# Performance work log

Hardware: AMD Instinct MI355X
Metric: run time of the kernel (lower is better)

## Reference

```python
import jax, jax.numpy as jnp
import numpy as np
from math import pi

B, L, S, D, H, M, DK, IND, KS = 8, 3072, 3072, 512, 8, 2, 64, 96, 25


def _linear(x, W, b):
    return x @ W + b


def _moving_avg(x, k):
    # Autoformer-style moving average with edge replication, stride 1.  x: [B, T, D]
    pad = (k - 1) // 2
    xp = jnp.concatenate([jnp.repeat(x[:, :1], pad, axis=1), x,
                          jnp.repeat(x[:, -1:], pad, axis=1)], axis=1)
    c = jnp.cumsum(xp, axis=1)
    c = jnp.concatenate([jnp.zeros_like(c[:, :1]), c], axis=1)
    return (c[:, k:] - c[:, :-k]) / k


def _trend_norm(x, g, b):
    # series_decomp(kernel=25): LayerNorm the seasonal part, add back the trend.
    trend = _moving_avg(x, KS)
    seas = x - trend
    mu = jnp.mean(seas, axis=-1, keepdims=True)
    var = jnp.var(seas, axis=-1, keepdims=True)
    return (seas - mu) * jax.lax.rsqrt(var + 1e-5) * g + b + trend


def _quat_attention(q, k, v, q_om, q_th, k_om, k_th):
    # q: [B,Lq,H,E]; k,v: [B,Sk,H,E]; omegas/thetas: [B,*,H,M]
    Bq, Lq, Hh, E = q.shape
    Sk = k.shape[1]
    Mm = q_om.shape[-1]
    qpos = (jnp.arange(Lq, dtype=q.dtype) / Lq)[None, :, None, None]
    kpos = (jnp.arange(Sk, dtype=q.dtype) / Sk)[None, :, None, None]
    Qa = q_om * qpos + q_th
    Ka = k_om * kpos + k_th
    Qc, Qs = jnp.cos(Qa), jnp.sin(Qa)
    Kc, Ks = jnp.cos(Ka), jnp.sin(Ka)
    q0, q1, q2, q3 = jnp.split(q, 4, axis=-1)
    k0, k1, k2, k3 = jnp.split(k, 4, axis=-1)
    op = lambda a, t: jnp.einsum('blhe,blhm->blhme', a, t)
    Qr = jnp.concatenate([op(q0, Qc) - op(q1, Qs), op(q1, Qc) + op(q0, Qs),
                          op(q2, Qc) + op(q3, Qs), op(q3, Qc) - op(q2, Qs)], axis=-1)
    Kr = jnp.concatenate([op(k0, Kc) - op(k2, Ks), op(k1, Kc) - op(k3, Ks),
                          op(k2, Kc) + op(k0, Ks), op(k3, Kc) + op(k1, Ks)], axis=-1)
    scores = jnp.einsum('blhme,bshme->bhls', Qr, Kr) / Mm
    scale = 1.0 / jnp.sqrt(jnp.asarray(E, q.dtype))
    A = jax.nn.softmax(scale * scores, axis=-1)
    return jnp.einsum('bhls,bshd->blhd', A, v)


def _ltr_layer(p, queries, keys, values):
    Bq, Lq, _ = queries.shape
    Sk = keys.shape[1]
    # kernel_size=1 convs == pointwise linears
    q_om = jax.nn.relu(_linear(queries, p['Wqo'], p['bqo'])).reshape(Bq, Lq, H, M)
    k_om = jax.nn.relu(_linear(keys, p['Wko'], p['bko'])).reshape(Bq, Sk, H, M)
    q_th = (jnp.tanh(_linear(queries, p['Wqt'], p['bqt'])) * pi).reshape(Bq, Lq, H, M)
    k_th = (jnp.tanh(_linear(keys, p['Wkt'], p['bkt'])) * pi).reshape(Bq, Sk, H, M)
    q = _linear(queries, p['Wq'], p['bq']).reshape(Bq, Lq, H, DK)
    k = _linear(keys, p['Wk'], p['bk']).reshape(Bq, Sk, H, DK)
    v = _linear(values, p['Wv'], p['bv']).reshape(Bq, Sk, H, DK)
    out = _quat_attention(q, k, v, q_om, q_th, k_om, k_th).reshape(Bq, Lq, H * DK)
    # D-matrix penalty == first-order difference along sequence
    om_pen = jnp.sum(jnp.diff(q_om, axis=1) ** 2) + jnp.sum(jnp.diff(k_om, axis=1) ** 2)
    th_pen = jnp.sum(q_th ** 2) + jnp.sum(k_th ** 2)
    return _linear(out, p['Wo'], p['bo']), om_pen, th_pen


def setup_inputs() -> dict:
    key = jax.random.key(0)
    ks = iter(jax.random.split(key, 32))
    rn = lambda shape, s=1.0: jax.random.normal(next(ks), shape, jnp.float32) * s
    w = 0.03  # ~1/sqrt(d_model)
    return dict(
        queries=rn((B, L, D)), keys=rn((B, S, D)), values=rn((B, S, D)),
        Wq=rn((2, D, D), w), bq=jnp.zeros((2, D), jnp.float32),
        Wk=rn((2, D, D), w), bk=jnp.zeros((2, D), jnp.float32),
        Wv=rn((2, D, D), w), bv=jnp.zeros((2, D), jnp.float32),
        Wqo=rn((2, D, M * H), w), bqo=jnp.zeros((2, M * H), jnp.float32),
        Wko=rn((2, D, M * H), w), bko=jnp.zeros((2, M * H), jnp.float32),
        Wqt=rn((2, D, M * H), w), bqt=jnp.zeros((2, M * H), jnp.float32),
        Wkt=rn((2, D, M * H), w), bkt=jnp.zeros((2, M * H), jnp.float32),
        Wo=rn((2, D, D), w), bo=jnp.zeros((2, D), jnp.float32),
        I=rn((1, IND, D), w),
        ln_g=jnp.ones((D,), jnp.float32), ln_b=jnp.zeros((D,), jnp.float32),
    )


def reference(queries, keys, values, Wq, bq, Wk, bk, Wv, bv, Wqo, bqo, Wko, bko,
              Wqt, bqt, Wkt, bkt, Wo, bo, I, ln_g, ln_b):
    def lp(i):
        return dict(Wq=Wq[i], bq=bq[i], Wk=Wk[i], bk=bk[i], Wv=Wv[i], bv=bv[i],
                    Wqo=Wqo[i], bqo=bqo[i], Wko=Wko[i], bko=bko[i],
                    Wqt=Wqt[i], bqt=bqt[i], Wkt=Wkt[i], bkt=bkt[i],
                    Wo=Wo[i], bo=bo[i])
    Bq = queries.shape[0]
    inducings = jnp.broadcast_to(I, (Bq, IND, D))
    inducings, om1, th1 = _ltr_layer(lp(0), inducings, keys, values)
    inducings = _trend_norm(inducings, ln_g, ln_b)
    out, om2, th2 = _ltr_layer(lp(1), queries, inducings, inducings)
    return out, om1 + om2, th1 + th2
```

## Files before the change

### kernel.cpp

```cpp
#include <hip/hip_runtime.h>
#include <math.h>

#define PI_F 3.14159265358979323846f

namespace {
constexpr int B_ = 8;
constexpr int L_ = 3072;
constexpr int S_ = 3072;
constexpr int H_ = 8;
constexpr int NF = 544;
constexpr int NSC = 8;
constexpr int SCHUNK = S_ / NSC;
}

typedef __attribute__((ext_vector_type(8))) short bf16x8;
typedef __attribute__((ext_vector_type(4))) float f32x4;

__device__ inline f32x4 mfma16(bf16x8 a, bf16x8 b, f32x4 c) {
  return __builtin_amdgcn_mfma_f32_16x16x32_bf16(a, b, c, 0, 0, 0);
}

__device__ inline ushort f2bf(float f) {
  union { float f; unsigned u; } v;
  v.f = f;
  unsigned r = v.u + 0x7FFFu + ((v.u >> 16) & 1u);
  return (ushort)(r >> 16);
}

__device__ inline void gl_lds16(const void* g, void* l) {
  __builtin_amdgcn_global_load_lds(
      (const __attribute__((address_space(1))) unsigned int*)g,
      (__attribute__((address_space(3))) unsigned int*)l, 16, 0, 0);
}

__device__ inline int xcd_swizzle(int flat, int nwg) {
  int q = nwg >> 3, r = nwg & 7;
  int xcd = flat & 7, ix = flat >> 3;
  return (xcd < r ? xcd * (q + 1) : r * (q + 1) + (xcd - r) * q) + ix;
}

__global__ void init_pen(float* pen) {
  if (threadIdx.x < 16) pen[threadIdx.x] = 0.f;
}

__global__ void write_pen(const float* __restrict__ pen, float* __restrict__ out) {
  if (threadIdx.x == 0) out[12582912] = pen[0];
  if (threadIdx.x == 1) out[12582913] = pen[1];
}

__global__ void pack_w(const float* __restrict__ Wm, const float* __restrict__ Wo_,
                       const float* __restrict__ Wt, const float* __restrict__ bm,
                       const float* __restrict__ bo_, const float* __restrict__ bt,
                       float* __restrict__ Wcat, float* __restrict__ bcat) {
  int gid = blockIdx.x * 256 + threadIdx.x;
  if (gid < 512 * 544) {
    int k = gid / 544, n = gid % 544;
    float v;
    if (n < 512) v = Wm[(size_t)k * 512 + n];
    else if (n < 528) v = Wo_[k * 16 + (n - 512)];
    else v = Wt[k * 16 + (n - 528)];
    Wcat[gid] = v;
  }
  if (gid < 544) {
    float v;
    if (gid < 512) v = bm[gid];
    else if (gid < 528) v = bo_[gid - 512];
    else v = bt[gid - 528];
    bcat[gid] = v;
  }
}

__global__ void pack_wt_fused(const float* __restrict__ Wm, const float* __restrict__ Wo_,
                              const float* __restrict__ Wt, const float* __restrict__ bm,
                              const float* __restrict__ bo_, const float* __restrict__ bt,
                              ushort* __restrict__ BT, float* __restrict__ bias) {
  int gid = blockIdx.x * 256 + threadIdx.x;
  if (gid < 640 * 512) {
    int n = gid >> 9, k = gid & 511;
    float v = 0.f;
    if (n < 512) v = Wm[(size_t)k * 512 + n];
    else if (n < 528) v = Wo_[k * 16 + (n - 512)];
    else if (n < 544) v = Wt[k * 16 + (n - 528)];
    BT[gid] = f2bf(v);
  }
  if (gid < 544)
    bias[gid] = (gid < 512) ? bm[gid] : (gid < 528 ? bo_[gid - 512] : bt[gid - 528]);
}

__global__ void pack_wt_plain(const float* __restrict__ W, const float* __restrict__ b,
                              ushort* __restrict__ BT, float* __restrict__ bias) {
  int gid = blockIdx.x * 256 + threadIdx.x;
  if (gid < 512 * 512) {
    int n = gid >> 9, k = gid & 511;
    BT[gid] = f2bf(W[(size_t)k * 512 + n]);
  }
  if (gid < 512) bias[gid] = b[gid];
}

__global__ __launch_bounds__(256)
void cast_bf16(const float* __restrict__ src, ushort* __restrict__ dst, int n8) {
  int gid = blockIdx.x * 256 + threadIdx.x;
  if (gid < n8) {
    float4 a = ((const float4*)src)[(size_t)gid * 2];
    float4 b = ((const float4*)src)[(size_t)gid * 2 + 1];
    ushort u[8] = {f2bf(a.x), f2bf(a.y), f2bf(a.z), f2bf(a.w),
                   f2bf(b.x), f2bf(b.y), f2bf(b.z), f2bf(b.w)};
    ((uint4*)dst)[gid] = *(uint4*)u;
  }
}

__global__ __launch_bounds__(256)
void gemm_bf16_mfma(const ushort* __restrict__ A, const ushort* __restrict__ BT,
                    const float* __restrict__ bias, float* __restrict__ C,
                    int ldc, int Nout, int act) {
  __shared__ ushort As[128][32];
  __shared__ ushort Bs[128][32];
  const int tid = threadIdx.x;
  const int wv = tid >> 6, lane = tid & 63, quad = lane >> 4, col = lane & 15;
  const int wm = wv & 1, wn = wv >> 1;

  const int nwg = gridDim.x * gridDim.y;
  const int flat = blockIdx.y * gridDim.x + blockIdx.x;
  const int nf = xcd_swizzle(flat, nwg);
  const int bx = nf % gridDim.x, by = nf / gridDim.x;
  const int m0 = by * 128, n0 = bx * 128;

  const int srow = lane >> 2;
  const int scol = (lane & 3) * 8;

  f32x4 acc[4][4];
#pragma unroll
  for (int i = 0; i < 4; ++i)
#pragma unroll
    for (int j = 0; j < 4; ++j) {
      f32x4 z = {0.f, 0.f, 0.f, 0.f};
      acc[i][j] = z;
    }

  const ushort* Ag = A + (size_t)(m0 + wv * 32) * 512;
  const ushort* Bg = BT + (size_t)(n0 + wv * 32) * 512;

  for (int k0 = 0; k0 < 512; k0 += 32) {
    __syncthreads();
    gl_lds16(Ag + (size_t)srow * 512 + k0 + scol, &As[wv * 32][0]);
    gl_lds16(Ag + (size_t)(srow + 16) * 512 + k0 + scol, &As[wv * 32 + 16][0]);
    gl_lds16(Bg + (size_t)srow * 512 + k0 + scol, &Bs[wv * 32][0]);
    gl_lds16(Bg + (size_t)(srow + 16) * 512 + k0 + scol, &Bs[wv * 32 + 16][0]);
    __syncthreads();
    bf16x8 av[4], bv[4];
#pragma unroll
    for (int mi = 0; mi < 4; ++mi)
      av[mi] = *(const bf16x8*)&As[wm * 64 + mi * 16 + col][quad * 8];
#pragma unroll
    for (int ni = 0; ni < 4; ++ni)
      bv[ni] = *(const bf16x8*)&Bs[wn * 64 + ni * 16 + col][quad * 8];
#pragma unroll
    for (int mi = 0; mi < 4; ++mi)
#pragma unroll
      for (int ni = 0; ni < 4; ++ni)
        acc[mi][ni] = mfma16(av[mi], bv[ni], acc[mi][ni]);
  }

#pragma unroll
  for (int mi = 0; mi < 4; ++mi) {
#pragma unroll
    for (int ni = 0; ni < 4; ++ni) {
      int n = n0 + wn * 64 + ni * 16 + col;
      if (n >= Nout) continue;
      float bs = bias[n];
#pragma unroll
      for (int r = 0; r < 4; ++r) {
        int m = m0 + wm * 64 + mi * 16 + quad * 4 + r;
        float v = acc[mi][ni][r] + bs;
        if (act && n >= 512) v = (n < 528) ? fmaxf(v, 0.f) : tanhf(v) * PI_F;
        C[(size_t)m * ldc + n] = v;
      }
    }
  }
}

__global__ __launch_bounds__(256)
void gemm_k512(const float* __restrict__ A, const float* __restrict__ W,
               const float* __restrict__ bias, float* __restrict__ C,
               int M, int N, int act) {
  __shared__ float As[16][68];
  __shared__ float Ws_[16][68];
  const int tid = threadIdx.x;
  const int tx = tid & 15, ty = tid >> 4;
  const int m0 = blockIdx.y * 64, n0 = blockIdx.x * 64;

  float acc[4][4];
#pragma unroll
  for (int i = 0; i < 4; ++i)
#pragma unroll
    for (int j = 0; j < 4; ++j) acc[i][j] = 0.f;

  const int arow = tid >> 2;
  const int acol4 = (tid & 3) * 4;
  const int wrow = tid >> 4;
  const int wcol4 = (tid & 15) * 4;

  for (int k0 = 0; k0 < 512; k0 += 16) {
    float4 av = make_float4(0.f, 0.f, 0.f, 0.f);
    int gm = m0 + arow;
    if (gm < M) av = *(const float4*)(A + (size_t)gm * 512 + k0 + acol4);
    As[acol4 + 0][arow] = av.x;
    As[acol4 + 1][arow] = av.y;
    As[acol4 + 2][arow] = av.z;
    As[acol4 + 3][arow] = av.w;
    float4 wv;
    int gn = n0 + wcol4;
    if (gn + 3 < N) {
      wv = *(const float4*)(W + (size_t)(k0 + wrow) * N + gn);
    } else {
      float tmp[4] = {0.f, 0.f, 0.f, 0.f};
      for (int u = 0; u < 4; ++u)
        if (gn + u < N) tmp[u] = W[(size_t)(k0 + wrow) * N + gn + u];
      wv = make_float4(tmp[0], tmp[1], tmp[2], tmp[3]);
    }
    *(float4*)&Ws_[wrow][wcol4] = wv;
    __syncthreads();
#pragma unroll
    for (int k = 0; k < 16; ++k) {
      float4 a4 = *(const float4*)&As[k][ty * 4];
      float4 b4 = *(const float4*)&Ws_[k][tx * 4];
      float a[4] = {a4.x, a4.y, a4.z, a4.w};
      float b[4] = {b4.x, b4.y, b4.z, b4.w};
#pragma unroll
      for (int i = 0; i < 4; ++i)
#pragma unroll
        for (int j = 0; j < 4; ++j) acc[i][j] = fmaf(a[i], b[j], acc[i][j]);
    }
    __syncthreads();
  }

#pragma unroll
  for (int i = 0; i < 4; ++i) {
    int gm = m0 + ty * 4 + i;
    if (gm >= M) continue;
#pragma unroll
    for (int j = 0; j < 4; ++j) {
      int gn = n0 + tx * 4 + j;
      if (gn >= N) continue;
      float v = acc[i][j] + bias[gn];
      if (act && gn >= 512) v = (gn < 528) ? fmaxf(v, 0.f) : tanhf(v) * PI_F;
      C[(size_t)gm * N + gn] = v;
    }
  }
}

__global__ __launch_bounds__(256)
void build_qr0(const float* __restrict__ QF0, ushort* __restrict__ Qr0bf) {
  const int l = blockIdx.x;
  const float* row = QF0 + (size_t)l * NF;
  __shared__ float2 trig[8][2];
  const int tid = threadIdx.x;
  if (tid < 16) {
    int h = tid >> 1, m = tid & 1;
    float om = row[512 + h * 2 + m], th = row[528 + h * 2 + m];
    float qa = fmaf(om, (float)l / 96.f, th);
    trig[h][m] = make_float2(cosf(qa), sinf(qa));
  }
  __syncthreads();
  for (int idx = tid; idx < 1024; idx += 256) {
    int h = idx >> 7, d = idx & 127;
    int m = d >> 6, r = d & 63, c = r >> 4, e = r & 15;
    float qc = row[h * 64 + c * 16 + e];
    float qp = row[h * 64 + (c ^ 1) * 16 + e];
    float2 tg = trig[h][m];
    float sgn = (c == 0 || c == 3) ? -1.f : 1.f;
    Qr0bf[((size_t)h * 96 + l) * 128 + d] = f2bf(fmaf(qc, tg.x, sgn * qp * tg.y));
  }
}

__global__ __launch_bounds__(256)
void build_kr0(const float* __restrict__ KF0, ushort* __restrict__ Kr0) {
  const int rs = blockIdx.x;
  const int b = rs / S_, s = rs - b * S_;
  const float* row = KF0 + (size_t)rs * NF;
  __shared__ float2 trig[8][2];
  const int tid = threadIdx.x;
  if (tid < 16) {
    int h = tid >> 1, m = tid & 1;
    float om = row[512 + h * 2 + m], th = row[528 + h * 2 + m];
    float ka = fmaf(om, (float)s * (1.f / (float)S_), th);
    trig[h][m] = make_float2(cosf(ka), sinf(ka));
  }
  __syncthreads();
  for (int idx = tid; idx < 512; idx += 256) {
    int h = idx >> 6, d = (idx & 63) * 2;
    int m = d >> 6, r = d & 63, c = r >> 4, e = r & 15;
    const float* rh = row + h * 64;
    float2 kc = *(const float2*)(rh + c * 16 + e);
    float2 kp = *(const float2*)(rh + (c ^ 2) * 16 + e);
    float2 tg = trig[h][m];
    float sgn = (c < 2) ? -1.f : 1.f;
    ushort2 u;
    u.x = f2bf(fmaf(kc.x, tg.x, sgn * kp.x * tg.y));
    u.y = f2bf(fmaf(kc.y, tg.x, sgn * kp.y * tg.y));
    *(ushort2*)&Kr0[(((size_t)(b * 8 + h)) * S_ + s) * 128 + d] = u;
  }
}

__global__ __launch_bounds__(256)
void build_vt0(const float* __restrict__ V0, ushort* __restrict__ Vt0) {
  const int st = blockIdx.x, h = blockIdx.y, b = blockIdx.z;
  const int s0 = st * 64;
  const int tid = threadIdx.x;
  __shared__ ushort T[64][68];
  for (int idx = tid; idx < 4096; idx += 256) {
    int s = idx >> 6, d = idx & 63;
    T[d][s] = f2bf(V0[((size_t)(b * S_ + s0 + s)) * 512 + h * 64 + d]);
  }
  __syncthreads();
  for (int idx = tid; idx < 2048; idx += 256) {
    int d = idx >> 5, s2 = (idx & 31) * 2;
    ushort2 u = *(const ushort2*)&T[d][s2];
    *(ushort2*)&Vt0[(((size_t)(b * 8 + h)) * 64 + d) * S_ + s0 + s2] = u;
  }
}

__global__ __launch_bounds__(256)
void build_kr1(const float* __restrict__ KF1, float* __restrict__ Kr1) {
  const int rs = blockIdx.x;
  const int b = rs / 96, s = rs % 96;
  const float* row = KF1 + (size_t)rs * NF;
  __shared__ float2 trig[8][2];
  const int tid = threadIdx.x;
  if (tid < 16) {
    int h = tid >> 1, m = tid & 1;
    float om = row[512 + h * 2 + m], th = row[528 + h * 2 + m];
    float ka = fmaf(om, (float)s / 96.f, th);
    trig[h][m] = make_float2(cosf(ka), sinf(ka));
  }
  __syncthreads();
  for (int idx = tid; idx < 1024; idx += 256) {
    int h = idx >> 7, d = idx & 127;
    int m = d >> 6, r = d & 63, c = r >> 4, e = r & 15;
    float kc = row[h * 64 + c * 16 + e];
    float kp = row[h * 64 + (c ^ 2) * 16 + e];
    float2 tg = trig[h][m];
    float sgn = (c < 2) ? -1.f : 1.f;
    Kr1[(((size_t)(b * 8 + h)) * 96 + s) * 128 + d] = fmaf(kc, tg.x, sgn * kp * tg.y);
  }
}

__global__ __launch_bounds__(256)
void attn0_mfma(const ushort* __restrict__ Kr0, const ushort* __restrict__ Vt0,
                const ushort* __restrict__ Qr0bf, float* __restrict__ accP,
                float* __restrict__ sumP) {
  const int sc = blockIdx.x, h = blockIdx.y, b = blockIdx.z;
  const int tid = threadIdx.x;
  const int wv = tid >> 6, lane = tid & 63, quad = lane >> 4, col = lane & 15;

  __shared__ __align__(16) ushort Qs[96][136];
  __shared__ __align__(16) ushort Ks[64][136];
  __shared__ __align__(16) ushort Vt[64][72];
  __shared__ __align__(16) ushort Ps[96][72];
  __shared__ float rowsum[96];

  const ushort* Qg = Qr0bf + (size_t)h * 96 * 128;
  for (int idx = tid; idx < 96 * 16; idx += 256) {
    int l = idx >> 4, c8 = (idx & 15) * 8;
    *(uint4*)&Qs[l][c8] = *(const uint4*)(Qg + (size_t)l * 128 + c8);
  }
  if (tid < 96) rowsum[tid] = 0.f;

  f32x4 oacc[6];
#pragma unroll
  for (int i = 0; i < 6; ++i) {
    f32x4 z = {0.f, 0.f, 0.f, 0.f};
    oacc[i] = z;
  }

  const int s0g = sc * SCHUNK;
  const ushort* Kb = Kr0 + ((size_t)(b * 8 + h) * S_ + s0g) * 128;
  const ushort* Vb = Vt0 + ((size_t)(b * 8 + h)) * 64 * S_ + s0g;

  for (int t = 0; t < 6; ++t) {
    __syncthreads();
    for (int idx = tid; idx < 64 * 16; idx += 256) {
      int s = idx >> 4, c8 = (idx & 15) * 8;
      *(uint4*)&Ks[s][c8] = *(const uint4*)(Kb + ((size_t)(t * 64 + s)) * 128 + c8);
    }
    for (int idx = tid; idx < 64 * 8; idx += 256) {
      int d = idx >> 3, c8 = (idx & 7) * 8;
      *(uint4*)&Vt[d][c8] = *(const uint4*)(Vb + (size_t)d * S_ + t * 64 + c8);
    }
    __syncthreads();
    bf16x8 bk[4];
#pragma unroll
    for (int k = 0; k < 4; ++k)
      bk[k] = *(const bf16x8*)&Ks[wv * 16 + col][k * 32 + quad * 8];
    f32x4 sacc[6];
#pragma unroll
    for (int mt = 0; mt < 6; ++mt) {
      f32x4 z = {0.f, 0.f, 0.f, 0.f};
      sacc[mt] = z;
#pragma unroll
      for (int k = 0; k < 4; ++k) {
        bf16x8 a = *(const bf16x8*)&Qs[mt * 16 + col][k * 32 + quad * 8];
        sacc[mt] = mfma16(a, bk[k], sacc[mt]);
      }
    }
#pragma unroll
    for (int mt = 0; mt < 6; ++mt) {
      float pr[4];
#pragma unroll
      for (int r = 0; r < 4; ++r) {
        float p = __expf(sacc[mt][r] * 0.0625f);
        pr[r] = p;
        Ps[mt * 16 + quad * 4 + r][wv * 16 + col] = f2bf(p);
      }
#pragma unroll
      for (int r = 0; r < 4; ++r) {
#pragma unroll
        for (int off = 1; off < 16; off <<= 1) pr[r] += __shfl_xor(pr[r], off);
      }
      if (col == 0) {
#pragma unroll
        for (int r = 0; r < 4; ++r)
          atomicAdd(&rowsum[mt * 16 + quad * 4 + r], pr[r]);
      }
    }
    __syncthreads();
    bf16x8 bv0 = *(const bf16x8*)&Vt[wv * 16 + col][quad * 8];
    bf16x8 bv1 = *(const bf16x8*)&Vt[wv * 16 + col][32 + quad * 8];
#pragma unroll
    for (int mt = 0; mt < 6; ++mt) {
      bf16x8 a0 = *(const bf16x8*)&Ps[mt * 16 + col][quad * 8];
      oacc[mt] = mfma16(a0, bv0, oacc[mt]);
      bf16x8 a1 = *(const bf16x8*)&Ps[mt * 16 + col][32 + quad * 8];
      oacc[mt] = mfma16(a1, bv1, oacc[mt]);
    }
  }
  __syncthreads();
  const size_t pbase = (((size_t)(b * 8 + h)) * NSC + sc) * 96;
#pragma unroll
  for (int mt = 0; mt < 6; ++mt) {
#pragma unroll
    for (int r = 0; r < 4; ++r) {
      int l = mt * 16 + quad * 4 + r;
      accP[(pbase + l) * 64 + wv * 16 + col] = oacc[mt][r];
    }
  }
  if (tid < 96) sumP[pbase + tid] = rowsum[tid];
}

__global__ __launch_bounds__(256)
void attn0_stage2(const float* __restrict__ accP, const float* __restrict__ sumP,
                  float* __restrict__ attn0) {
  const int l = blockIdx.x, b = blockIdx.y;
  const int tid = threadIdx.x;
  for (int e = tid; e < 512; e += 256) {
    int h = e >> 6, d = e & 63;
    size_t base = ((size_t)(b * 8 + h)) * NSC * 96;
    float num = 0.f, den = 0.f;
    for (int scv = 0; scv < NSC; ++scv) {
      size_t pb = base + (size_t)scv * 96 + l;
      num += accP[pb * 64 + d];
      den += sumP[pb];
    }
    attn0[((size_t)(b * 96 + l)) * 512 + e] = num / den;
  }
}

__global__ __launch_bounds__(256)
void trend_norm(const float* __restrict__ y, const float* __restrict__ g,
                const float* __restrict__ be, float* __restrict__ outp) {
  const int t = blockIdx.x, b = blockIdx.y;
  const int tid = threadIdx.x;
  __shared__ float red[256];
  __shared__ float red2[256];
  float seas[2], trend[2];
  float lsum = 0.f, lsum2 = 0.f;
#pragma unroll
  for (int u = 0; u < 2; ++u) {
    int d = tid + u * 256;
    float tr = 0.f;
    for (int j = -12; j <= 12; ++j) {
      int tt = t + j;
      tt = tt < 0 ? 0 : (tt > 95 ? 95 : tt);
      tr += y[((size_t)(b * 96 + tt)) * 512 + d];
    }
    tr *= (1.f / 25.f);
    float x = y[((size_t)(b * 96 + t)) * 512 + d];
    float se = x - tr;
    seas[u] = se;
    trend[u] = tr;
    lsum += se;
    lsum2 += se * se;
  }
  red[tid] = lsum;
  red2[tid] = lsum2;
  __syncthreads();
  for (int off = 128; off > 0; off >>= 1) {
    if (tid < off) {
      red[tid] += red[tid + off];
      red2[tid] += red2[tid + off];
    }
    __syncthreads();
  }
  float mu = red[0] / 512.f;
  float var = red2[0] / 512.f - mu * mu;
  float rs = rsqrtf(var + 1e-5f);
#pragma unroll
  for (int u = 0; u < 2; ++u) {
    int d = tid + u * 256;
    outp[((size_t)(b * 96 + t)) * 512 + d] = (seas[u] - mu) * rs * g[d] + be[d] + trend[u];
  }
}

__global__ __launch_bounds__(256)
void penalty(const float* __restrict__ base, int R, int nb, float mult,
             float* __restrict__ pen) {
  const int tid = threadIdx.x;
  size_t gid = (size_t)blockIdx.x * 256 + tid;
  size_t total = (size_t)nb * R * 16;
  float omv = 0.f, thv = 0.f;
  if (gid < total) {
    int j = (int)(gid & 15);
    size_t row = gid >> 4;
    int s = (int)(row % R);
    const float* r0 = base + row * NF;
    float th = r0[528 + j];
    thv = th * th;
    if (s < R - 1) {
      float d = r0[NF + 512 + j] - r0[512 + j];
      omv = d * d;
    }
  }
  __shared__ float ro[256], rt[256];
  ro[tid] = omv;
  rt[tid] = thv;
  __syncthreads();
  for (int off = 128; off > 0; off >>= 1) {
    if (tid < off) {
      ro[tid] += ro[tid + off];
      rt[tid] += rt[tid + off];
    }
    __syncthreads();
  }
  if (tid == 0) {
    atomicAdd(pen + 0, mult * ro[0]);
    atomicAdd(pen + 1, mult * rt[0]);
  }
}

__global__ __launch_bounds__(256)
void attn1_mfma(const float* __restrict__ QF1, const float* __restrict__ Kr1,
                const float* __restrict__ V1, ushort* __restrict__ attn1) {
  const int nwg = gridDim.x * gridDim.y * gridDim.z;
  const int flat = (blockIdx.z * gridDim.y + blockIdx.y) * gridDim.x + blockIdx.x;
  const int nf = xcd_swizzle(flat, nwg);
  const int lt = nf % gridDim.x;
  const int rest = nf / gridDim.x;
  const int h = rest % gridDim.y, b = rest / gridDim.y;
  const int l0 = lt * 64;
  const int tid = threadIdx.x;
  const int wv = tid >> 6, lane = tid & 63, quad = lane >> 4, col = lane & 15;

  __shared__ __align__(16) ushort Qs[64][136];
  __shared__ __align__(16) ushort Ks[96][136];
  __shared__ __align__(16) ushort Vt[64][104];
  __shared__ __align__(16) ushort Ps[64][104];
  __shared__ float2 trigq[64][2];

  if (tid < 128) {
    int l = tid >> 1, m = tid & 1;
    const float* row = QF1 + (size_t)(b * L_ + l0 + l) * NF;
    float om = row[512 + h * 2 + m];
    float th = row[528 + h * 2 + m];
    float qa = fmaf(om, (float)(l0 + l) * (1.f / (float)L_), th);
    trigq[l][m] = make_float2(cosf(qa), sinf(qa));
  }
  __syncthreads();
  for (int idx = tid; idx < 64 * 128; idx += 256) {
    int l = idx >> 7, d = idx & 127;
    int m = d >> 6, r = d & 63, c = r >> 4, e = r & 15;
    const float* row = QF1 + (size_t)(b * L_ + l0 + l) * NF + h * 64;
    float qc = row[c * 16 + e];
    float qp = row[(c ^ 1) * 16 + e];
    float2 tg = trigq[l][m];
    float sgn = (c == 0 || c == 3) ? -1.f : 1.f;
    Qs[l][d] = f2bf(fmaf(qc, tg.x, sgn * qp * tg.y));
  }
  const float* Krb = Kr1 + (size_t)(b * 8 + h) * 96 * 128;
  for (int idx = tid; idx < 96 * 64; idx += 256) {
    int s = idx >> 6, d2 = (idx & 63) * 2;
    float2 kk = *(const float2*)(Krb + (size_t)s * 128 + d2);
    ushort2 u;
    u.x = f2bf(kk.x);
    u.y = f2bf(kk.y);
    *(ushort2*)&Ks[s][d2] = u;
  }
  for (int idx = tid; idx < 96 * 64; idx += 256) {
    int s = idx >> 6, d = idx & 63;
    Vt[d][s] = f2bf(V1[(size_t)(b * 96 + s) * 512 + h * 64 + d]);
  }
  __syncthreads();

  bf16x8 aq[4];
#pragma unroll
  for (int k = 0; k < 4; ++k)
    aq[k] = *(const bf16x8*)&Qs[wv * 16 + col][k * 32 + quad * 8];
  f32x4 sacc[6];
#pragma unroll
  for (int nt = 0; nt < 6; ++nt) {
    f32x4 z = {0.f, 0.f, 0.f, 0.f};
    sacc[nt] = z;
#pragma unroll
    for (int k = 0; k < 4; ++k) {
      bf16x8 bkf = *(const bf16x8*)&Ks[nt * 16 + col][k * 32 + quad * 8];
      sacc[nt] = mfma16(aq[k], bkf, sacc[nt]);
    }
  }
  float rsum[4] = {0.f, 0.f, 0.f, 0.f};
#pragma unroll
  for (int nt = 0; nt < 6; ++nt) {
#pragma unroll
    for (int r = 0; r < 4; ++r) {
      float p = __expf(sacc[nt][r] * 0.0625f);
      Ps[wv * 16 + quad * 4 + r][nt * 16 + col] = f2bf(p);
      rsum[r] += p;
    }
  }
#pragma unroll
  for (int r = 0; r < 4; ++r) {
#pragma unroll
    for (int off = 1; off < 16; off <<= 1) rsum[r] += __shfl_xor(rsum[r], off);
  }
  __syncthreads();
  bf16x8 ap[3];
#pragma unroll
  for (int kt = 0; kt < 3; ++kt)
    ap[kt] = *(const bf16x8*)&Ps[wv * 16 + col][kt * 32 + quad * 8];
  f32x4 oacc[4];
#pragma unroll
  for (int nt = 0; nt < 4; ++nt) {
    f32x4 z = {0.f, 0.f, 0.f, 0.f};
    oacc[nt] = z;
#pragma unroll
    for (int kt = 0; kt < 3; ++kt) {
      bf16x8 bvf = *(const bf16x8*)&Vt[nt * 16 + col][kt * 32 + quad * 8];
      oacc[nt] = mfma16(ap[kt], bvf, oacc[nt]);
    }
  }
  float inv[4];
#pragma unroll
  for (int r = 0; r < 4; ++r) inv[r] = 1.f / rsum[r];
#pragma unroll
  for (int nt = 0; nt < 4; ++nt) {
#pragma unroll
    for (int r = 0; r < 4; ++r) {
      int l = wv * 16 + quad * 4 + r;
      attn1[(size_t)(b * L_ + l0 + l) * 512 + h * 64 + nt * 16 + col] =
          f2bf(oacc[nt][r] * inv[r]);
    }
  }
}

extern "C" void kernel_launch(void* const* d_in, const int* in_sizes, int n_in,
                              void* d_out, int out_size, void* d_ws, size_t ws_size,
                              hipStream_t stream) {
  (void)in_sizes; (void)n_in; (void)out_size; (void)ws_size;
  const float* queries = (const float*)d_in[0];
  const float* keys = (const float*)d_in[1];
  const float* values = (const float*)d_in[2];
  const float* Wq = (const float*)d_in[3];
  const float* bq = (const float*)d_in[4];
  const float* Wk = (const float*)d_in[5];
  const float* bk = (const float*)d_in[6];
  const float* Wv = (const float*)d_in[7];
  const float* bv = (const float*)d_in[8];
  const float* Wqo = (const float*)d_in[9];
  const float* bqo = (const float*)d_in[10];
  const float* Wko = (const float*)d_in[11];
  const float* bko = (const float*)d_in[12];
  const float* Wqt = (const float*)d_in[13];
  const float* bqt = (const float*)d_in[14];
  const float* Wkt = (const float*)d_in[15];
  const float* bkt = (const float*)d_in[16];
  const float* Wo = (const float*)d_in[17];
  const float* bo = (const float*)d_in[18];
  const float* I = (const float*)d_in[19];
  const float* ln_g = (const float*)d_in[20];
  const float* ln_b = (const float*)d_in[21];
  float* out = (float*)d_out;

  float* ws = (float*)d_ws;
  size_t off = 0;
  auto alloc = [&](size_t n) {
    float* p = ws + off;
    off += (n + 3) & ~(size_t)3;
    return p;
  };
  auto allocU = [&](size_t n) { return (ushort*)alloc((n + 1) / 2); };

  float* WCAT0Q = alloc(512 * 544);
  float* WCAT1K = alloc(512 * 544);
  float* BCAT0Q = alloc(544);
  float* BCAT1K = alloc(544);
  ushort* BT0K = allocU(640 * 512);
  ushort* BT1Q = allocU(640 * 512);
  ushort* BTV0 = allocU(512 * 512);
  ushort* BTO1 = allocU(512 * 512);
  float* B0K = alloc(544);
  float* B1Q = alloc(544);
  float* BV0 = alloc(512);
  float* BO1 = alloc(512);
  float* pen = alloc(16);
  float* QF0 = alloc(96 * 544);
  ushort* Qr0bf = allocU(8 * 96 * 128);
  float* KF0 = alloc((size_t)24576 * 544);
  float* V0 = alloc((size_t)24576 * 512);
  float* attn0 = alloc(768 * 512);
  float* y0 = alloc(768 * 512);
  float* xind = alloc(768 * 512);
  float* KF1 = alloc(768 * 544);
  float* V1 = alloc(768 * 512);
  float* Kr1 = alloc((size_t)64 * 96 * 128);
  float* accP = alloc((size_t)64 * NSC * 96 * 64);
  float* sumP = alloc((size_t)64 * NSC * 96);
  ushort* XB1 = allocU((size_t)24576 * 512);
  ushort* XB2 = allocU((size_t)24576 * 512);
  ushort* Kr0U = XB1;
  ushort* Vt0U = allocU((size_t)64 * 64 * S_);
  float* QF1 = KF0;

  init_pen<<<1, 64, 0, stream>>>(pen);
  const int packBlocks = (512 * 544 + 255) / 256;
  pack_w<<<packBlocks, 256, 0, stream>>>(Wq, Wqo, Wqt, bq, bqo, bqt, WCAT0Q, BCAT0Q);
  pack_w<<<packBlocks, 256, 0, stream>>>(Wk + 262144, Wko + 8192, Wkt + 8192,
                                         bk + 512, bko + 16, bkt + 16, WCAT1K, BCAT1K);
  pack_wt_fused<<<(640 * 512 + 255) / 256, 256, 0, stream>>>(
      Wk, Wko, Wkt, bk, bko, bkt, BT0K, B0K);
  pack_wt_fused<<<(640 * 512 + 255) / 256, 256, 0, stream>>>(
      Wq + 262144, Wqo + 8192, Wqt + 8192, bq + 512, bqo + 16, bqt + 16, BT1Q, B1Q);
  pack_wt_plain<<<(512 * 512 + 255) / 256, 256, 0, stream>>>(Wv, bv, BTV0, BV0);
  pack_wt_plain<<<(512 * 512 + 255) / 256, 256, 0, stream>>>(Wo + 262144, bo + 512,
                                                             BTO1, BO1);
  const int castBlocks = (24576 * 512 / 8 + 255) / 256;
  cast_bf16<<<castBlocks, 256, 0, stream>>>(keys, XB1, 24576 * 512 / 8);
  cast_bf16<<<castBlocks, 256, 0, stream>>>(values, XB2, 24576 * 512 / 8);

  gemm_bf16_mfma<<<dim3(5, 192), 256, 0, stream>>>(XB1, BT0K, B0K, KF0, 544, 544, 1);
  gemm_bf16_mfma<<<dim3(4, 192), 256, 0, stream>>>(XB2, BTV0, BV0, V0, 512, 512, 0);
  gemm_k512<<<dim3(9, 2), 256, 0, stream>>>(I, WCAT0Q, BCAT0Q, QF0, 96, 544, 1);
  build_qr0<<<96, 256, 0, stream>>>(QF0, Qr0bf);
  penalty<<<(96 * 16 + 255) / 256, 256, 0, stream>>>(QF0, 96, 1, 8.f, pen);
  penalty<<<(24576 * 16 + 255) / 256, 256, 0, stream>>>(KF0, 3072, 8, 1.f, pen);
  build_kr0<<<24576, 256, 0, stream>>>(KF0, Kr0U);
  build_vt0<<<dim3(48, 8, 8), 256, 0, stream>>>(V0, Vt0U);
  attn0_mfma<<<dim3(8, 8, 8), 256, 0, stream>>>(Kr0U, Vt0U, Qr0bf, accP, sumP);
  attn0_stage2<<<dim3(96, 8), 256, 0, stream>>>(accP, sumP, attn0);
  gemm_k512<<<dim3(8, 12), 256, 0, stream>>>(attn0, Wo, bo, y0, 768, 512, 0);
  trend_norm<<<dim3(96, 8), 256, 0, stream>>>(y0, ln_g, ln_b, xind);

  gemm_k512<<<dim3(9, 12), 256, 0, stream>>>(xind, WCAT1K, BCAT1K, KF1, 768, 544, 1);
  gemm_k512<<<dim3(8, 12), 256, 0, stream>>>(xind, Wv + 262144, bv + 512, V1, 768, 512, 0);
  build_kr1<<<768, 256, 0, stream>>>(KF1, Kr1);
  penalty<<<(768 * 16 + 255) / 256, 256, 0, stream>>>(KF1, 96, 8, 1.f, pen);
  cast_bf16<<<castBlocks, 256, 0, stream>>>(queries, XB1, 24576 * 512 / 8);
  gemm_bf16_mfma<<<dim3(5, 192), 256, 0, stream>>>(XB1, BT1Q, B1Q, QF1, 544, 544, 1);
  penalty<<<(24576 * 16 + 255) / 256, 256, 0, stream>>>(QF1, 3072, 8, 1.f, pen);
  attn1_mfma<<<dim3(48, 8, 8), 256, 0, stream>>>(QF1, Kr1, V1, XB2);
  gemm_bf16_mfma<<<dim3(4, 192), 256, 0, stream>>>(XB2, BTO1, BO1, out, 512, 512, 0);
  write_pen<<<1, 64, 0, stream>>>(pen, out);
}
```

Before: 772.2 us.

## Precompute bf16 rotated Q/K and transposed V; read MFMA operands directly from global

Moves the quaternion rotation of Q for the second attention into a separate build_qr1 kernel that writes bf16, makes build_kr1 emit bf16, and adds build_vt1 to pre-transpose V1 to bf16. Both attention kernels drop their LDS staging of K and V (and Q for attn1) and load MFMA fragments straight from global memory, removing shared-memory copies and one barrier per tile. The trade-off is an extra pass over QF1 and uncoalesced, cache-dependent global fragment loads in place of staged LDS reads. Qr1 reuses the V0 buffer, which is safe because V0 is no longer needed at that point.

```diff
diff --git a/kernel.cpp b/kernel.cpp
--- a/kernel.cpp
+++ b/kernel.cpp
@@ -321,7 +321,7 @@
 }
 
 __global__ __launch_bounds__(256)
-void build_kr1(const float* __restrict__ KF1, float* __restrict__ Kr1) {
+void build_kr1(const float* __restrict__ KF1, ushort* __restrict__ Kr1b) {
   const int rs = blockIdx.x;
   const int b = rs / 96, s = rs % 96;
   const float* row = KF1 + (size_t)rs * NF;
@@ -334,14 +334,63 @@
     trig[h][m] = make_float2(cosf(ka), sinf(ka));
   }
   __syncthreads();
-  for (int idx = tid; idx < 1024; idx += 256) {
-    int h = idx >> 7, d = idx & 127;
+  for (int idx = tid; idx < 512; idx += 256) {
+    int h = idx >> 6, d = (idx & 63) * 2;
     int m = d >> 6, r = d & 63, c = r >> 4, e = r & 15;
-    float kc = row[h * 64 + c * 16 + e];
-    float kp = row[h * 64 + (c ^ 2) * 16 + e];
+    const float* rh = row + h * 64;
+    float2 kc = *(const float2*)(rh + c * 16 + e);
+    float2 kp = *(const float2*)(rh + (c ^ 2) * 16 + e);
     float2 tg = trig[h][m];
     float sgn = (c < 2) ? -1.f : 1.f;
-    Kr1[(((size_t)(b * 8 + h)) * 96 + s) * 128 + d] = fmaf(kc, tg.x, sgn * kp * tg.y);
+    ushort2 u;
+    u.x = f2bf(fmaf(kc.x, tg.x, sgn * kp.x * tg.y));
+    u.y = f2bf(fmaf(kc.y, tg.x, sgn * kp.y * tg.y));
+    *(ushort2*)&Kr1b[(((size_t)(b * 8 + h)) * 96 + s) * 128 + d] = u;
+  }
+}
+
+__global__ __launch_bounds__(256)
+void build_qr1(const float* __restrict__ QF1, ushort* __restrict__ Qr1) {
+  const int rl = blockIdx.x;
+  const int b = rl / L_, l = rl - b * L_;
+  const float* row = QF1 + (size_t)rl * NF;
+  __shared__ float2 trig[8][2];
+  const int tid = threadIdx.x;
+  if (tid < 16) {
+    int h = tid >> 1, m = tid & 1;
+    float om = row[512 + h * 2 + m], th = row[528 + h * 2 + m];
+    float qa = fmaf(om, (float)l * (1.f / (float)L_), th);
+    trig[h][m] = make_float2(cosf(qa), sinf(qa));
+  }
+  __syncthreads();
+  for (int idx = tid; idx < 512; idx += 256) {
+    int h = idx >> 6, d = (idx & 63) * 2;
+    int m = d >> 6, r = d & 63, c = r >> 4, e = r & 15;
+    const float* rh = row + h * 64;
+    float2 qc = *(const float2*)(rh + c * 16 + e);
+    float2 qp = *(const float2*)(rh + (c ^ 1) * 16 + e);
+    float2 tg = trig[h][m];
+    float sgn = (c == 0 || c == 3) ? -1.f : 1.f;
+    ushort2 u;
+    u.x = f2bf(fmaf(qc.x, tg.x, sgn * qp.x * tg.y));
+    u.y = f2bf(fmaf(qc.y, tg.x, sgn * qp.y * tg.y));
+    *(ushort2*)&Qr1[(((size_t)(b * 8 + h)) * L_ + l) * 128 + d] = u;
+  }
+}
+
+__global__ __launch_bounds__(256)
+void build_vt1(const float* __restrict__ V1, ushort* __restrict__ Vt1) {
+  const int h = blockIdx.x, b = blockIdx.y;
+  const int tid = threadIdx.x;
+  __shared__ ushort T[64][104];
+  for (int idx = tid; idx < 96 * 64; idx += 256) {
+    int s = idx >> 6, d = idx & 63;
+    T[d][s] = f2bf(V1[(size_t)(b * 96 + s) * 512 + h * 64 + d]);
+  }
+  __syncthreads();
+  for (int idx = tid; idx < 64 * 12; idx += 256) {
+    int d = idx / 12, c8 = (idx % 12) * 8;
+    *(uint4*)&Vt1[(((size_t)(b * 8 + h)) * 64 + d) * 96 + c8] = *(const uint4*)&T[d][c8];
   }
 }
 
@@ -354,8 +403,6 @@
   const int wv = tid >> 6, lane = tid & 63, quad = lane >> 4, col = lane & 15;
 
   __shared__ __align__(16) ushort Qs[96][136];
-  __shared__ __align__(16) ushort Ks[64][136];
-  __shared__ __align__(16) ushort Vt[64][72];
   __shared__ __align__(16) ushort Ps[96][72];
   __shared__ float rowsum[96];
 
@@ -377,21 +424,14 @@
   const ushort* Kb = Kr0 + ((size_t)(b * 8 + h) * S_ + s0g) * 128;
   const ushort* Vb = Vt0 + ((size_t)(b * 8 + h)) * 64 * S_ + s0g;
 
+  __syncthreads();
+
   for (int t = 0; t < 6; ++t) {
-    __syncthreads();
-    for (int idx = tid; idx < 64 * 16; idx += 256) {
-      int s = idx >> 4, c8 = (idx & 15) * 8;
-      *(uint4*)&Ks[s][c8] = *(const uint4*)(Kb + ((size_t)(t * 64 + s)) * 128 + c8);
-    }
-    for (int idx = tid; idx < 64 * 8; idx += 256) {
-      int d = idx >> 3, c8 = (idx & 7) * 8;
-      *(uint4*)&Vt[d][c8] = *(const uint4*)(Vb + (size_t)d * S_ + t * 64 + c8);
-    }
-    __syncthreads();
+    const ushort* Kt = Kb + ((size_t)(t * 64 + wv * 16 + col)) * 128;
     bf16x8 bk[4];
 #pragma unroll
     for (int k = 0; k < 4; ++k)
-      bk[k] = *(const bf16x8*)&Ks[wv * 16 + col][k * 32 + quad * 8];
+      bk[k] = *(const bf16x8*)(Kt + k * 32 + quad * 8);
     f32x4 sacc[6];
 #pragma unroll
     for (int mt = 0; mt < 6; ++mt) {
@@ -424,8 +464,9 @@
       }
     }
     __syncthreads();
-    bf16x8 bv0 = *(const bf16x8*)&Vt[wv * 16 + col][quad * 8];
-    bf16x8 bv1 = *(const bf16x8*)&Vt[wv * 16 + col][32 + quad * 8];
+    const ushort* Vt = Vb + ((size_t)(wv * 16 + col)) * S_ + t * 64;
+    bf16x8 bv0 = *(const bf16x8*)(Vt + quad * 8);
+    bf16x8 bv1 = *(const bf16x8*)(Vt + 32 + quad * 8);
 #pragma unroll
     for (int mt = 0; mt < 6; ++mt) {
       bf16x8 a0 = *(const bf16x8*)&Ps[mt * 16 + col][quad * 8];
@@ -433,8 +474,8 @@
       bf16x8 a1 = *(const bf16x8*)&Ps[mt * 16 + col][32 + quad * 8];
       oacc[mt] = mfma16(a1, bv1, oacc[mt]);
     }
-  }
-  __syncthreads();
+    __syncthreads();
+  }
   const size_t pbase = (((size_t)(b * 8 + h)) * NSC + sc) * 96;
 #pragma unroll
   for (int mt = 0; mt < 6; ++mt) {
@@ -548,8 +589,8 @@
 }
 
 __global__ __launch_bounds__(256)
-void attn1_mfma(const float* __restrict__ QF1, const float* __restrict__ Kr1,
-                const float* __restrict__ V1, ushort* __restrict__ attn1) {
+void attn1_mfma(const ushort* __restrict__ Qr1, const ushort* __restrict__ Kr1b,
+                const ushort* __restrict__ Vt1, ushort* __restrict__ attn1) {
   const int nwg = gridDim.x * gridDim.y * gridDim.z;
   const int flat = (blockIdx.z * gridDim.y + blockIdx.y) * gridDim.x + blockIdx.x;
   const int nf = xcd_swizzle(flat, nwg);
@@ -560,50 +601,17 @@
   const int tid = threadIdx.x;
   const int wv = tid >> 6, lane = tid & 63, quad = lane >> 4, col = lane & 15;
 
-  __shared__ __align__(16) ushort Qs[64][136];
-  __shared__ __align__(16) ushort Ks[96][136];
-  __shared__ __align__(16) ushort Vt[64][104];
   __shared__ __align__(16) ushort Ps[64][104];
-  __shared__ float2 trigq[64][2];
-
-  if (tid < 128) {
-    int l = tid >> 1, m = tid & 1;
-    const float* row = QF1 + (size_t)(b * L_ + l0 + l) * NF;
-    float om = row[512 + h * 2 + m];
-    float th = row[528 + h * 2 + m];
-    float qa = fmaf(om, (float)(l0 + l) * (1.f / (float)L_), th);
-    trigq[l][m] = make_float2(cosf(qa), sinf(qa));
-  }
-  __syncthreads();
-  for (int idx = tid; idx < 64 * 128; idx += 256) {
-    int l = idx >> 7, d = idx & 127;
-    int m = d >> 6, r = d & 63, c = r >> 4, e = r & 15;
-    const float* row = QF1 + (size_t)(b * L_ + l0 + l) * NF + h * 64;
-    float qc = row[c * 16 + e];
-    float qp = row[(c ^ 1) * 16 + e];
-    float2 tg = trigq[l][m];
-    float sgn = (c == 0 || c == 3) ? -1.f : 1.f;
-    Qs[l][d] = f2bf(fmaf(qc, tg.x, sgn * qp * tg.y));
-  }
-  const float* Krb = Kr1 + (size_t)(b * 8 + h) * 96 * 128;
-  for (int idx = tid; idx < 96 * 64; idx += 256) {
-    int s = idx >> 6, d2 = (idx & 63) * 2;
-    float2 kk = *(const float2*)(Krb + (size_t)s * 128 + d2);
-    ushort2 u;
-    u.x = f2bf(kk.x);
-    u.y = f2bf(kk.y);
-    *(ushort2*)&Ks[s][d2] = u;
-  }
-  for (int idx = tid; idx < 96 * 64; idx += 256) {
-    int s = idx >> 6, d = idx & 63;
-    Vt[d][s] = f2bf(V1[(size_t)(b * 96 + s) * 512 + h * 64 + d]);
-  }
-  __syncthreads();
+
+  const ushort* Qg = Qr1 + ((size_t)(b * 8 + h) * L_ + l0) * 128;
+  const ushort* Kg = Kr1b + (size_t)(b * 8 + h) * 96 * 128;
+  const ushort* Vg = Vt1 + (size_t)(b * 8 + h) * 64 * 96;
 
   bf16x8 aq[4];
 #pragma unroll
   for (int k = 0; k < 4; ++k)
-    aq[k] = *(const bf16x8*)&Qs[wv * 16 + col][k * 32 + quad * 8];
+    aq[k] = *(const bf16x8*)(Qg + ((size_t)(wv * 16 + col)) * 128 + k * 32 + quad * 8);
+
   f32x4 sacc[6];
 #pragma unroll
   for (int nt = 0; nt < 6; ++nt) {
@@ -611,7 +619,8 @@
     sacc[nt] = z;
 #pragma unroll
     for (int k = 0; k < 4; ++k) {
-      bf16x8 bkf = *(const bf16x8*)&Ks[nt * 16 + col][k * 32 + quad * 8];
+      bf16x8 bkf =
+          *(const bf16x8*)(Kg + ((size_t)(nt * 16 + col)) * 128 + k * 32 + quad * 8);
       sacc[nt] = mfma16(aq[k], bkf, sacc[nt]);
     }
   }
@@ -642,7 +651,8 @@
     oacc[nt] = z;
 #pragma unroll
     for (int kt = 0; kt < 3; ++kt) {
-      bf16x8 bvf = *(const bf16x8*)&Vt[nt * 16 + col][kt * 32 + quad * 8];
+      bf16x8 bvf =
+          *(const bf16x8*)(Vg + ((size_t)(nt * 16 + col)) * 96 + kt * 32 + quad * 8);
       oacc[nt] = mfma16(ap[kt], bvf, oacc[nt]);
     }
   }
@@ -719,7 +729,8 @@
   float* xind = alloc(768 * 512);
   float* KF1 = alloc(768 * 544);
   float* V1 = alloc(768 * 512);
-  float* Kr1 = alloc((size_t)64 * 96 * 128);
+  ushort* Kr1b = allocU((size_t)64 * 96 * 128);
+  ushort* Vt1 = allocU((size_t)64 * 64 * 96);
   float* accP = alloc((size_t)64 * NSC * 96 * 64);
   float* sumP = alloc((size_t)64 * NSC * 96);
   ushort* XB1 = allocU((size_t)24576 * 512);
@@ -727,6 +738,7 @@
   ushort* Kr0U = XB1;
   ushort* Vt0U = allocU((size_t)64 * 64 * S_);
   float* QF1 = KF0;
+  ushort* Qr1U = (ushort*)V0;
 
   init_pen<<<1, 64, 0, stream>>>(pen);
   const int packBlocks = (512 * 544 + 255) / 256;
@@ -759,12 +771,14 @@
 
   gemm_k512<<<dim3(9, 12), 256, 0, stream>>>(xind, WCAT1K, BCAT1K, KF1, 768, 544, 1);
   gemm_k512<<<dim3(8, 12), 256, 0, stream>>>(xind, Wv + 262144, bv + 512, V1, 768, 512, 0);
-  build_kr1<<<768, 256, 0, stream>>>(KF1, Kr1);
+  build_kr1<<<768, 256, 0, stream>>>(KF1, Kr1b);
+  build_vt1<<<dim3(8, 8), 256, 0, stream>>>(V1, Vt1);
   penalty<<<(768 * 16 + 255) / 256, 256, 0, stream>>>(KF1, 96, 8, 1.f, pen);
   cast_bf16<<<castBlocks, 256, 0, stream>>>(queries, XB1, 24576 * 512 / 8);
   gemm_bf16_mfma<<<dim3(5, 192), 256, 0, stream>>>(XB1, BT1Q, B1Q, QF1, 544, 544, 1);
   penalty<<<(24576 * 16 + 255) / 256, 256, 0, stream>>>(QF1, 3072, 8, 1.f, pen);
-  attn1_mfma<<<dim3(48, 8, 8), 256, 0, stream>>>(QF1, Kr1, V1, XB2);
+  build_qr1<<<24576, 256, 0, stream>>>(QF1, Qr1U);
+  attn1_mfma<<<dim3(48, 8, 8), 256, 0, stream>>>(Qr1U, Kr1b, Vt1, XB2);
   gemm_bf16_mfma<<<dim3(4, 192), 256, 0, stream>>>(XB2, BTO1, BO1, out, 512, 512, 0);
   write_pen<<<1, 64, 0, stream>>>(pen, out);
 }
```

After: 773.4 us. Within noise of the previous version (+0.2%).
